# Kernel tuning notes

Measured on AMD Instinct MI355X. Metric: run time of the kernel, lower is better.

The kernel has to match this reference:

```python
import jax, jax.numpy as jnp
import numpy as np

N_NODES = 100000
E_EDGES = 1600000
F_DIM = 48
AVG_LOG = float(np.log(17.0))  # avg_deg['log'] for avg degree 16
EPS = 1e-5  # PNA std epsilon


def setup_inputs() -> dict:
    key = jax.random.key(0)
    k1, k2, k3 = jax.random.split(key, 3)
    x = jax.random.normal(k1, (E_EDGES, F_DIM), dtype=jnp.float32)
    index = jax.random.randint(k2, (E_EDGES,), 0, N_NODES, dtype=jnp.int32)
    w = jax.random.normal(k3, (12,), dtype=jnp.float32)  # post_pn: Linear(12 -> 1, bias=False)
    return {"x": x, "index": index, "dim_size": N_NODES, "w": w}


def reference(x, index, dim_size, w):
    # degree per target node [N]
    deg = jax.ops.segment_sum(jnp.ones(index.shape, x.dtype), index, num_segments=dim_size)
    safe_deg = jnp.maximum(deg, 1.0)[:, None]  # avoid /0 for empty segments

    # single-pass stats: sum and sum of squares -> mean, std
    s = jax.ops.segment_sum(x, index, num_segments=dim_size)          # [N,F]
    sq = jax.ops.segment_sum(x * x, index, num_segments=dim_size)     # [N,F]
    mean = s / safe_deg
    var = jnp.maximum(sq / safe_deg - mean * mean, 0.0)
    std = jnp.sqrt(var + EPS)

    mn = jax.ops.segment_min(x, index, num_segments=dim_size)
    mx = jax.ops.segment_max(x, index, num_segments=dim_size)
    nonempty = (deg > 0.0)[:, None]
    mn = jnp.where(nonempty, mn, 0.0)  # torch_scatter fills empty segments with 0
    mx = jnp.where(nonempty, mx, 0.0)

    aggs = jnp.stack([mean, mn, mx, std], axis=-1)  # [N,F,4]

    logdeg = jnp.log(deg + 1.0)
    amp = logdeg / AVG_LOG                               # amplification scaler
    att = jnp.where(deg > 0.0, AVG_LOG / jnp.where(deg > 0.0, logdeg, 1.0), 0.0)  # attenuation
    scalers = jnp.stack([jnp.ones_like(deg), amp, att], axis=-1)  # [N,3]

    # loop order in torch: aggregator outer, scaler inner -> [N,F,4,3] -> [N,F,12]
    out12 = (aggs[:, :, :, None] * scalers[:, None, None, :]).reshape(dim_size, F_DIM, 12)
    out = jnp.einsum('nfk,k->nf', out12, w)  # post_pn then squeeze
    return out
```

## Files before the change

kernel.cpp:

```cpp
#include <hip/hip_runtime.h>
#include <math.h>

#define N_NODES 100000
#define E_EDGES 1600000
#define F_DIM   48
#define NF      (N_NODES * F_DIM)
#define AVG_LOG 2.8332133440562162f
#define PNA_EPS 1e-5f
#define CAP     64

typedef float f32x4 __attribute__((ext_vector_type(4)));

__global__ void k_zero(unsigned* __restrict__ cnt) {
    int i = blockIdx.x * blockDim.x + threadIdx.x;
    if (i < N_NODES) cnt[i] = 0u;
}

__global__ void k_fill(const int4* __restrict__ index4, unsigned* __restrict__ cnt,
                       unsigned* __restrict__ eids) {
    int t = blockIdx.x * blockDim.x + threadIdx.x;
    if (t >= E_EDGES / 4) return;
    int4 idx = index4[t];
    unsigned e0 = (unsigned)t * 4u;

    unsigned p0 = atomicAdd(&cnt[idx.x], 1u);
    if (p0 < CAP) eids[(unsigned)idx.x * CAP + p0] = e0 + 0u;
    unsigned p1 = atomicAdd(&cnt[idx.y], 1u);
    if (p1 < CAP) eids[(unsigned)idx.y * CAP + p1] = e0 + 1u;
    unsigned p2 = atomicAdd(&cnt[idx.z], 1u);
    if (p2 < CAP) eids[(unsigned)idx.z * CAP + p2] = e0 + 2u;
    unsigned p3 = atomicAdd(&cnt[idx.w], 1u);
    if (p3 < CAP) eids[(unsigned)idx.w * CAP + p3] = e0 + 3u;
}

__global__ __launch_bounds__(256) void k_reduce(const f32x4* __restrict__ x4,
                                                const unsigned* __restrict__ eids,
                                                const unsigned* __restrict__ cnt,
                                                const float* __restrict__ w,
                                                float* __restrict__ out) {
    int t = blockIdx.x * blockDim.x + threadIdx.x;
    if (t >= N_NODES * 12) return;
    int n = t / 12;
    int g = t - n * 12;

    const unsigned* eb  = eids + (unsigned)n * CAP;
    const uint4*    eb4 = (const uint4*)eb;
    unsigned d = cnt[n];
    if (d > CAP) d = CAP;

    float sx = 0.f, sy = 0.f, sz = 0.f, sw = 0.f;
    float qx = 0.f, qy = 0.f, qz = 0.f, qw = 0.f;
    float mnx =  INFINITY, mny =  INFINITY, mnz =  INFINITY, mnw =  INFINITY;
    float mxx = -INFINITY, mxy = -INFINITY, mxz = -INFINITY, mxw = -INFINITY;

#define ACC(v)                                                                 \
    do {                                                                       \
        sx += (v)[0]; sy += (v)[1]; sz += (v)[2]; sw += (v)[3];                \
        qx += (v)[0] * (v)[0]; qy += (v)[1] * (v)[1];                          \
        qz += (v)[2] * (v)[2]; qw += (v)[3] * (v)[3];                          \
        mnx = fminf(mnx, (v)[0]); mny = fminf(mny, (v)[1]);                    \
        mnz = fminf(mnz, (v)[2]); mnw = fminf(mnw, (v)[3]);                    \
        mxx = fmaxf(mxx, (v)[0]); mxy = fmaxf(mxy, (v)[1]);                    \
        mxz = fmaxf(mxz, (v)[2]); mxw = fmaxf(mxw, (v)[3]);                    \
    } while (0)

    unsigned i = 0;
    for (; i + 8 <= d; i += 8) {
        uint4 a = eb4[i >> 2];
        uint4 b = eb4[(i >> 2) + 1];
        f32x4 v0 = __builtin_nontemporal_load(&x4[a.x * 12u + (unsigned)g]);
        f32x4 v1 = __builtin_nontemporal_load(&x4[a.y * 12u + (unsigned)g]);
        f32x4 v2 = __builtin_nontemporal_load(&x4[a.z * 12u + (unsigned)g]);
        f32x4 v3 = __builtin_nontemporal_load(&x4[a.w * 12u + (unsigned)g]);
        f32x4 v4 = __builtin_nontemporal_load(&x4[b.x * 12u + (unsigned)g]);
        f32x4 v5 = __builtin_nontemporal_load(&x4[b.y * 12u + (unsigned)g]);
        f32x4 v6 = __builtin_nontemporal_load(&x4[b.z * 12u + (unsigned)g]);
        f32x4 v7 = __builtin_nontemporal_load(&x4[b.w * 12u + (unsigned)g]);
        ACC(v0); ACC(v1); ACC(v2); ACC(v3); ACC(v4); ACC(v5); ACC(v6); ACC(v7);
    }
    for (; i + 4 <= d; i += 4) {
        uint4 a = eb4[i >> 2];
        f32x4 v0 = __builtin_nontemporal_load(&x4[a.x * 12u + (unsigned)g]);
        f32x4 v1 = __builtin_nontemporal_load(&x4[a.y * 12u + (unsigned)g]);
        f32x4 v2 = __builtin_nontemporal_load(&x4[a.z * 12u + (unsigned)g]);
        f32x4 v3 = __builtin_nontemporal_load(&x4[a.w * 12u + (unsigned)g]);
        ACC(v0); ACC(v1); ACC(v2); ACC(v3);
    }
    for (; i < d; ++i) {
        unsigned e = eb[i];
        f32x4 v = __builtin_nontemporal_load(&x4[e * 12u + (unsigned)g]);
        ACC(v);
    }
#undef ACC

    float df = (float)d;
    float sd = fmaxf(df, 1.0f);
    float inv = 1.0f / sd;

    if (d == 0u) {
        mnx = mny = mnz = mnw = 0.f;
        mxx = mxy = mxz = mxw = 0.f;
    }

    float logdeg = logf(df + 1.0f);
    float amp = logdeg * (1.0f / AVG_LOG);
    float att = (d > 0u) ? (AVG_LOG / logdeg) : 0.0f;

    float c_mean = w[0] + w[1]  * amp + w[2]  * att;
    float c_min  = w[3] + w[4]  * amp + w[5]  * att;
    float c_max  = w[6] + w[7]  * amp + w[8]  * att;
    float c_std  = w[9] + w[10] * amp + w[11] * att;

    f32x4 o;
    {
        float mean = sx * inv;
        float var  = fmaxf(qx * inv - mean * mean, 0.0f);
        o[0] = mean * c_mean + mnx * c_min + mxx * c_max + sqrtf(var + PNA_EPS) * c_std;
    }
    {
        float mean = sy * inv;
        float var  = fmaxf(qy * inv - mean * mean, 0.0f);
        o[1] = mean * c_mean + mny * c_min + mxy * c_max + sqrtf(var + PNA_EPS) * c_std;
    }
    {
        float mean = sz * inv;
        float var  = fmaxf(qz * inv - mean * mean, 0.0f);
        o[2] = mean * c_mean + mnz * c_min + mxz * c_max + sqrtf(var + PNA_EPS) * c_std;
    }
    {
        float mean = sw * inv;
        float var  = fmaxf(qw * inv - mean * mean, 0.0f);
        o[3] = mean * c_mean + mnw * c_min + mxw * c_max + sqrtf(var + PNA_EPS) * c_std;
    }

    ((f32x4*)out)[n * 12 + g] = o;
}

extern "C" void kernel_launch(void* const* d_in, const int* in_sizes, int n_in,
                              void* d_out, int out_size, void* d_ws, size_t ws_size,
                              hipStream_t stream) {
    const f32x4* x4    = (const f32x4*)d_in[0];
    const int4*  index4 = (const int4*)d_in[1];
    const float* w     = (const float*)d_in[3];
    float* out = (float*)d_out;

    char* ws = (char*)d_ws;
    unsigned* cnt  = (unsigned*)(ws);
    unsigned* eids = (unsigned*)(ws + (size_t)N_NODES * 4);

    const int B = 256;
    k_zero<<<(N_NODES + B - 1) / B, B, 0, stream>>>(cnt);
    k_fill<<<(E_EDGES / 4 + B - 1) / B, B, 0, stream>>>(index4, cnt, eids);
    k_reduce<<<(N_NODES * 12 + B - 1) / B, B, 0, stream>>>(x4, eids, cnt, w, out);
}
```

Measured before the change: 224.1 us.

## Simplify fill to one edge per thread, drop nontemporal loads and 8-unroll

The zeroing kernel is replaced by hipMemsetAsync. The fill kernel now handles one edge per thread with scalar index loads instead of four edges per thread. The reduce kernel drops the 8-wide unrolled gather loop and uses ordinary cached loads instead of nontemporal loads for x. Normal caching lets rows of x that are gathered by the 12 threads of a node hit in cache, at the cost of less memory-level parallelism per thread.

```diff
diff --git a/kernel.cpp b/kernel.cpp
--- a/kernel.cpp
+++ b/kernel.cpp
@@ -11,26 +11,13 @@
 
 typedef float f32x4 __attribute__((ext_vector_type(4)));
 
-__global__ void k_zero(unsigned* __restrict__ cnt) {
-    int i = blockIdx.x * blockDim.x + threadIdx.x;
-    if (i < N_NODES) cnt[i] = 0u;
-}
-
-__global__ void k_fill(const int4* __restrict__ index4, unsigned* __restrict__ cnt,
+__global__ void k_fill(const int* __restrict__ index, unsigned* __restrict__ cnt,
                        unsigned* __restrict__ eids) {
-    int t = blockIdx.x * blockDim.x + threadIdx.x;
-    if (t >= E_EDGES / 4) return;
-    int4 idx = index4[t];
-    unsigned e0 = (unsigned)t * 4u;
-
-    unsigned p0 = atomicAdd(&cnt[idx.x], 1u);
-    if (p0 < CAP) eids[(unsigned)idx.x * CAP + p0] = e0 + 0u;
-    unsigned p1 = atomicAdd(&cnt[idx.y], 1u);
-    if (p1 < CAP) eids[(unsigned)idx.y * CAP + p1] = e0 + 1u;
-    unsigned p2 = atomicAdd(&cnt[idx.z], 1u);
-    if (p2 < CAP) eids[(unsigned)idx.z * CAP + p2] = e0 + 2u;
-    unsigned p3 = atomicAdd(&cnt[idx.w], 1u);
-    if (p3 < CAP) eids[(unsigned)idx.w * CAP + p3] = e0 + 3u;
+    int e = blockIdx.x * blockDim.x + threadIdx.x;
+    if (e >= E_EDGES) return;
+    int node = index[e];
+    unsigned pos = atomicAdd(&cnt[node], 1u);
+    if (pos < CAP) eids[(unsigned)node * CAP + pos] = (unsigned)e;
 }
 
 __global__ __launch_bounds__(256) void k_reduce(const f32x4* __restrict__ x4,
@@ -65,30 +52,17 @@
     } while (0)
 
     unsigned i = 0;
-    for (; i + 8 <= d; i += 8) {
-        uint4 a = eb4[i >> 2];
-        uint4 b = eb4[(i >> 2) + 1];
-        f32x4 v0 = __builtin_nontemporal_load(&x4[a.x * 12u + (unsigned)g]);
-        f32x4 v1 = __builtin_nontemporal_load(&x4[a.y * 12u + (unsigned)g]);
-        f32x4 v2 = __builtin_nontemporal_load(&x4[a.z * 12u + (unsigned)g]);
-        f32x4 v3 = __builtin_nontemporal_load(&x4[a.w * 12u + (unsigned)g]);
-        f32x4 v4 = __builtin_nontemporal_load(&x4[b.x * 12u + (unsigned)g]);
-        f32x4 v5 = __builtin_nontemporal_load(&x4[b.y * 12u + (unsigned)g]);
-        f32x4 v6 = __builtin_nontemporal_load(&x4[b.z * 12u + (unsigned)g]);
-        f32x4 v7 = __builtin_nontemporal_load(&x4[b.w * 12u + (unsigned)g]);
-        ACC(v0); ACC(v1); ACC(v2); ACC(v3); ACC(v4); ACC(v5); ACC(v6); ACC(v7);
-    }
     for (; i + 4 <= d; i += 4) {
         uint4 a = eb4[i >> 2];
-        f32x4 v0 = __builtin_nontemporal_load(&x4[a.x * 12u + (unsigned)g]);
-        f32x4 v1 = __builtin_nontemporal_load(&x4[a.y * 12u + (unsigned)g]);
-        f32x4 v2 = __builtin_nontemporal_load(&x4[a.z * 12u + (unsigned)g]);
-        f32x4 v3 = __builtin_nontemporal_load(&x4[a.w * 12u + (unsigned)g]);
+        f32x4 v0 = x4[a.x * 12u + (unsigned)g];
+        f32x4 v1 = x4[a.y * 12u + (unsigned)g];
+        f32x4 v2 = x4[a.z * 12u + (unsigned)g];
+        f32x4 v3 = x4[a.w * 12u + (unsigned)g];
         ACC(v0); ACC(v1); ACC(v2); ACC(v3);
     }
     for (; i < d; ++i) {
         unsigned e = eb[i];
-        f32x4 v = __builtin_nontemporal_load(&x4[e * 12u + (unsigned)g]);
+        f32x4 v = x4[e * 12u + (unsigned)g];
         ACC(v);
     }
 #undef ACC
@@ -140,7 +114,7 @@
                               void* d_out, int out_size, void* d_ws, size_t ws_size,
                               hipStream_t stream) {
     const f32x4* x4    = (const f32x4*)d_in[0];
-    const int4*  index4 = (const int4*)d_in[1];
+    const int*   index = (const int*)d_in[1];
     const float* w     = (const float*)d_in[3];
     float* out = (float*)d_out;
 
@@ -149,7 +123,7 @@
     unsigned* eids = (unsigned*)(ws + (size_t)N_NODES * 4);
 
     const int B = 256;
-    k_zero<<<(N_NODES + B - 1) / B, B, 0, stream>>>(cnt);
-    k_fill<<<(E_EDGES / 4 + B - 1) / B, B, 0, stream>>>(index4, cnt, eids);
+    hipMemsetAsync(cnt, 0, (size_t)N_NODES * 4, stream);
+    k_fill<<<(E_EDGES + B - 1) / B, B, 0, stream>>>(index, cnt, eids);
     k_reduce<<<(N_NODES * 12 + B - 1) / B, B, 0, stream>>>(x4, eids, cnt, w, out);
 }
```

After: 209.2 us. 1.07x faster.
